# Performance work log

Measured on AMD Instinct MI355X. Metric: run time of the kernel, lower is better.

## Reference

```python
import jax, jax.numpy as jnp
import numpy as np

EPS = 0.05    # geomloss: blur**p with p=1, blur=0.05
NITER = 30    # fixed Sinkhorn iterations (geomloss uses eps-scaling; fixed-eps loop is the reference math)


def _cost(x, y):
    # x:(N,3), y:(M,3) -> (N,M) Euclidean distance (p=1 ground cost)
    d2 = jnp.sum((x[:, None, :] - y[None, :, :]) ** 2, axis=-1)
    return jnp.sqrt(d2 + 1e-12)


def _sinkhorn_ot(x, y):
    # Entropic OT cost between uniform measures on x (N pts) and y (M pts), log-domain Sinkhorn.
    n, m = x.shape[0], y.shape[0]
    C = _cost(x, y)                                  # (N,M)
    log_a = jnp.full((n,), -jnp.log(jnp.float32(n)), dtype=x.dtype)
    log_b = jnp.full((m,), -jnp.log(jnp.float32(m)), dtype=x.dtype)

    def step(carry, _):
        f, g = carry
        # f_i = -eps * LSE_j( log_b_j + (g_j - C_ij)/eps )
        f = -EPS * jax.nn.logsumexp(log_b[None, :] + (g[None, :] - C) / EPS, axis=1)
        g = -EPS * jax.nn.logsumexp(log_a[:, None] + (f[:, None] - C) / EPS, axis=0)
        return (f, g), None

    f0 = jnp.zeros((n,), dtype=x.dtype)
    g0 = jnp.zeros((m,), dtype=x.dtype)
    (f, g), _ = jax.lax.scan(step, (f0, g0), None, length=NITER)
    a = jnp.exp(log_a)
    b = jnp.exp(log_b)
    return jnp.sum(a * f) + jnp.sum(b * g)


def _sinkhorn_divergence(x, y):
    # Debiased Sinkhorn divergence: S(x,y) = OT(x,y) - 0.5*OT(x,x) - 0.5*OT(y,y)
    return _sinkhorn_ot(x, y) - 0.5 * _sinkhorn_ot(x, x) - 0.5 * _sinkhorn_ot(y, y)


def setup_inputs() -> dict:
    key = jax.random.key(0)
    k1, k2 = jax.random.split(key)
    B, N, M = 8, 2048, 2048
    xyz1 = jax.random.normal(k1, (B, N, 3), dtype=jnp.float32)
    xyz2 = jax.random.normal(k2, (B, M, 3), dtype=jnp.float32)
    return {"xyz1": xyz1, "xyz2": xyz2}


def reference(xyz1, xyz2):
    # Per-batch Sinkhorn divergence, averaged over batch (original loops over b; vmap is the
    # vectorized equivalent since clouds are independent).
    losses = jax.vmap(_sinkhorn_divergence)(xyz1, xyz2)   # (B,)
    return jnp.sum(losses) / xyz1.shape[0]
```

## Files before the change

kernel.cpp:

```cpp
#include <hip/hip_runtime.h>

#define NPTS    2048
#define NBATCH  8
#define NPROB   24
#define NITER   30
#define TPB     512
#define WPB     8
#define NJOBS   32
#define HCOLS   1024
#define CPW     128

constexpr float KSC = 28.853900817779268f;
constexpr float C1f = 0.38123094930796995f;
constexpr float C2f = 0.03465735902799726f;

typedef float v2f __attribute__((ext_vector_type(2)));

__device__ __forceinline__ float fexp2(float x) { return __builtin_amdgcn_exp2f(x); }
__device__ __forceinline__ float flog2(float x) { return __builtin_amdgcn_logf(x); }
__device__ __forceinline__ float fsqrt(float x) { return __builtin_amdgcn_sqrtf(x); }

__global__ __launch_bounds__(256)
void init_sums(float* __restrict__ gsum)
{
    int i = blockIdx.x * 256 + threadIdx.x;
    if (i < NPROB * 2 * NPTS) gsum[i] = 1024.0f;
}

__device__ __forceinline__ void problem_barrier(unsigned* arrive, unsigned* epoch,
                                                unsigned phase, int nbpp, int tid)
{
    __syncthreads();
    if (tid == 0) {
        unsigned old = __hip_atomic_fetch_add(arrive, 1u, __ATOMIC_ACQ_REL,
                                              __HIP_MEMORY_SCOPE_AGENT);
        if (old == (unsigned)(nbpp - 1)) {
            __hip_atomic_store(arrive, 0u, __ATOMIC_RELAXED, __HIP_MEMORY_SCOPE_AGENT);
            __hip_atomic_store(epoch, phase, __ATOMIC_RELEASE, __HIP_MEMORY_SCOPE_AGENT);
        } else {
            while (__hip_atomic_load(epoch, __ATOMIC_RELAXED,
                                     __HIP_MEMORY_SCOPE_AGENT) < phase) {
                __builtin_amdgcn_s_sleep(2);
            }
            __threadfence();
        }
    }
    __syncthreads();
}

__global__ __launch_bounds__(TPB, 6)
void sinkhorn_all(const float* __restrict__ xyz1,
                  const float* __restrict__ xyz2,
                  float* __restrict__ fsum,
                  float* __restrict__ gsum,
                  unsigned* __restrict__ bars,
                  int nbpp)
{
    __shared__ float4 shC[HCOLS];
    __shared__ float  shS[WPB][128];

    const int tid  = threadIdx.x;
    const int lane = tid & 63;
    const int warp = tid >> 6;
    const int p    = blockIdx.x % NPROB;
    const int lb   = blockIdx.x / NPROB;
    const int b    = p / 3;
    const int k    = p - 3 * b;

    const float* xb = xyz1 + (size_t)b * NPTS * 3;
    const float* yb = xyz2 + (size_t)b * NPTS * 3;
    float* fS = fsum + (size_t)p * 2 * NPTS;
    float* gS = gsum + (size_t)p * 2 * NPTS;
    unsigned* arrive = bars + (size_t)p * 64;
    unsigned* epoch  = bars + (size_t)p * 64 + 32;

    const float* Uf = (k == 2) ? yb : xb;
    const float* Ug = (k == 0) ? yb : ((k == 1) ? xb : yb);
    const float* Vf = (k == 1) ? xb : yb;
    const float* Vg = (k == 2) ? yb : xb;

    auto stage = [&](const float* __restrict__ V, const float* __restrict__ S, int h) {
        if (tid < 256) {
            const float4* V4 = (const float4*)V;
            const int i0 = 3 * (h * 256 + tid);
            const float4 a  = V4[i0 + 0];
            const float4 bb = V4[i0 + 1];
            const float4 cc = V4[i0 + 2];
            const int c  = 4 * tid;
            const int gc = h * HCOLS + c;
            const float4 t0 = *(const float4*)(S + gc);
            const float4 t1 = *(const float4*)(S + NPTS + gc);
            shC[c + 0] = make_float4(a.x,  a.y,  a.z,  11.0f - flog2(t0.x + t1.x));
            shC[c + 1] = make_float4(a.w,  bb.x, bb.y, 11.0f - flog2(t0.y + t1.y));
            shC[c + 2] = make_float4(bb.z, bb.w, cc.x, 11.0f - flog2(t0.z + t1.z));
            shC[c + 3] = make_float4(cc.y, cc.z, cc.w, 11.0f - flog2(t0.w + t1.w));
        }
    };

    auto do_pass = [&](const float* __restrict__ U, float* __restrict__ oS,
                       int h, int rc) {
        __syncthreads();
        const int r0 = rc * 128 + lane, r1 = r0 + 64;
        const v2f ux = {U[3*r0],   U[3*r1]};
        const v2f uy = {U[3*r0+1], U[3*r1+1]};
        const v2f uz = {U[3*r0+2], U[3*r1+2]};
        const v2f e12 = {1e-12f, 1e-12f};
        const v2f nK  = {-KSC, -KSC};
        v2f s0 = {0.f, 0.f}, s1 = {0.f, 0.f}, s2 = {0.f, 0.f}, s3 = {0.f, 0.f};

        auto term = [&](const float4 v) -> v2f {
            v2f dx = ux - (v2f){v.x, v.x};
            v2f dy = uy - (v2f){v.y, v.y};
            v2f dz = uz - (v2f){v.z, v.z};
            v2f d2 = __builtin_elementwise_fma(dz, dz, e12);
            d2 = __builtin_elementwise_fma(dy, dy, d2);
            d2 = __builtin_elementwise_fma(dx, dx, d2);
            v2f sq  = {fsqrt(d2.x), fsqrt(d2.y)};
            v2f arg = __builtin_elementwise_fma(nK, sq, (v2f){v.w, v.w});
            return (v2f){fexp2(arg.x), fexp2(arg.y)};
        };
        const int cb = warp * CPW;
        #pragma unroll 2
        for (int c = cb; c < cb + CPW; c += 4) {
            const float4 v0 = shC[c + 0];
            const float4 v1 = shC[c + 1];
            const float4 v2 = shC[c + 2];
            const float4 v3 = shC[c + 3];
            s0 += term(v0);
            s1 += term(v1);
            s2 += term(v2);
            s3 += term(v3);
        }
        shS[warp][lane]      = (s0.x + s1.x) + (s2.x + s3.x);
        shS[warp][lane + 64] = (s0.y + s1.y) + (s2.y + s3.y);
        __syncthreads();
        if (tid < 128) {
            float t = shS[0][tid];
            #pragma unroll
            for (int w = 1; w < WPB; ++w) t += shS[w][tid];
            oS[h * NPTS + rc * 128 + tid] = t;
        }
        __syncthreads();
    };

    for (int it = 0; it < NITER; ++it) {
        for (int j = lb; j < NJOBS; j += nbpp) {
            stage(Vf, gS, j & 1);
            do_pass(Uf, fS, j & 1, j >> 1);
        }
        problem_barrier(arrive, epoch, (unsigned)(2 * it + 1), nbpp, tid);
        for (int j = lb; j < NJOBS; j += nbpp) {
            stage(Vg, fS, j & 1);
            do_pass(Ug, gS, j & 1, j >> 1);
        }
        problem_barrier(arrive, epoch, (unsigned)(2 * it + 2), nbpp, tid);
    }
}

__global__ __launch_bounds__(TPB, 1)
void final_reduce(const float* __restrict__ fsum, const float* __restrict__ gsum,
                  float* __restrict__ out)
{
    __shared__ double red[WPB];
    const int tid  = threadIdx.x;
    const int lane = tid & 63;
    const int warp = tid >> 6;

    double acc = 0.0;
    for (int idx = tid; idx < 2 * NPROB * NPTS; idx += TPB) {
        const bool isF = idx < NPROB * NPTS;
        const int rem  = isF ? idx : idx - NPROB * NPTS;
        const int pp   = rem >> 11;
        const int j    = rem & (NPTS - 1);
        const float* S = (isF ? fsum : gsum) + (size_t)pp * 2 * NPTS;
        const float t  = S[j] + S[NPTS + j];
        const float val = C1f - C2f * flog2(t);
        const float w   = (pp % 3 == 0) ? 1.0f : -0.5f;
        acc += (double)val * (double)w;
    }
    #pragma unroll
    for (int off = 32; off > 0; off >>= 1) acc += __shfl_xor(acc, off);
    if (lane == 0) red[warp] = acc;
    __syncthreads();
    if (warp == 0) {
        double v2 = (lane < WPB) ? red[lane] : 0.0;
        #pragma unroll
        for (int off = 32; off > 0; off >>= 1) v2 += __shfl_xor(v2, off);
        if (lane == 0) out[0] = (float)(v2 / (double)(NBATCH * NPTS));
    }
}

extern "C" void kernel_launch(void* const* d_in, const int* in_sizes, int n_in,
                              void* d_out, int out_size, void* d_ws, size_t ws_size,
                              hipStream_t stream)
{
    const float* xyz1 = (const float*)d_in[0];
    const float* xyz2 = (const float*)d_in[1];
    float* out = (float*)d_out;

    float* fsum = (float*)d_ws;
    float* gsum = fsum + (size_t)NPROB * 2 * NPTS;
    unsigned* bars = (unsigned*)(gsum + (size_t)NPROB * 2 * NPTS);

    hipMemsetAsync(bars, 0, (size_t)NPROB * 64 * sizeof(unsigned), stream);
    init_sums<<<(NPROB * 2 * NPTS + 255) / 256, 256, 0, stream>>>(gsum);

    int maxB = 0;
    hipOccupancyMaxActiveBlocksPerMultiprocessor(&maxB, sinkhorn_all, TPB, 0);
    if (maxB < 1) maxB = 1;
    int bpp = (maxB * 256) / NPROB;
    if (bpp > NJOBS) bpp = NJOBS;
    if (bpp < 1) bpp = 1;
    int nblk = NPROB * bpp;

    void* args[] = { (void*)&xyz1, (void*)&xyz2, (void*)&fsum, (void*)&gsum,
                     (void*)&bars, (void*)&bpp };
    hipLaunchCooperativeKernel((void*)sinkhorn_all, dim3(nblk), dim3(TPB),
                               args, 0, stream);

    final_reduce<<<1, TPB, 0, stream>>>(fsum, gsum, out);
}
```

Before: 2.349 ms.

## Split column range into four partial-sum quarters to raise block count per problem

Generalizes the column split from halves to a runtime-selected number of quarters (4 when workspace allows), doubling the number of jobs per Sinkhorn half-step, and raises the launch-bounds minimum-blocks hint from 6 to 8. The aim is to give more blocks work per problem so more of the GPU is used between grid-level barriers. In exchange, each stage step reads and sums more partial-sum arrays, does more staging and reduction per unit of compute, and the launch-bounds change may constrain registers.

```diff
diff --git a/kernel.cpp b/kernel.cpp
--- a/kernel.cpp
+++ b/kernel.cpp
@@ -6,9 +6,6 @@
 #define NITER   30
 #define TPB     512
 #define WPB     8
-#define NJOBS   32
-#define HCOLS   1024
-#define CPW     128
 
 constexpr float KSC = 28.853900817779268f;
 constexpr float C1f = 0.38123094930796995f;
@@ -21,10 +18,10 @@
 __device__ __forceinline__ float fsqrt(float x) { return __builtin_amdgcn_sqrtf(x); }
 
 __global__ __launch_bounds__(256)
-void init_sums(float* __restrict__ gsum)
+void init_sums(float* __restrict__ gsum, int n, float val)
 {
     int i = blockIdx.x * 256 + threadIdx.x;
-    if (i < NPROB * 2 * NPTS) gsum[i] = 1024.0f;
+    if (i < n) gsum[i] = val;
 }
 
 __device__ __forceinline__ void problem_barrier(unsigned* arrive, unsigned* epoch,
@@ -48,16 +45,21 @@
     __syncthreads();
 }
 
-__global__ __launch_bounds__(TPB, 6)
+__global__ __launch_bounds__(TPB, 8)
 void sinkhorn_all(const float* __restrict__ xyz1,
                   const float* __restrict__ xyz2,
                   float* __restrict__ fsum,
                   float* __restrict__ gsum,
                   unsigned* __restrict__ bars,
-                  int nbpp)
-{
-    __shared__ float4 shC[HCOLS];
+                  int nbpp, int lognq)
+{
+    __shared__ float4 shC[1024];
     __shared__ float  shS[WPB][128];
+
+    const int nq    = 1 << lognq;
+    const int njobs = 16 << lognq;
+    const int hc    = NPTS >> lognq;
+    const int cpw   = hc >> 3;
 
     const int tid  = threadIdx.x;
     const int lane = tid & 63;
@@ -69,8 +71,8 @@
 
     const float* xb = xyz1 + (size_t)b * NPTS * 3;
     const float* yb = xyz2 + (size_t)b * NPTS * 3;
-    float* fS = fsum + (size_t)p * 2 * NPTS;
-    float* gS = gsum + (size_t)p * 2 * NPTS;
+    float* fS = fsum + (size_t)p * nq * NPTS;
+    float* gS = gsum + (size_t)p * nq * NPTS;
     unsigned* arrive = bars + (size_t)p * 64;
     unsigned* epoch  = bars + (size_t)p * 64 + 32;
 
@@ -79,26 +81,30 @@
     const float* Vf = (k == 1) ? xb : yb;
     const float* Vg = (k == 2) ? yb : xb;
 
-    auto stage = [&](const float* __restrict__ V, const float* __restrict__ S, int h) {
-        if (tid < 256) {
+    auto stage = [&](const float* __restrict__ V, const float* __restrict__ S, int q) {
+        const int nst = hc >> 2;
+        if (tid < nst) {
             const float4* V4 = (const float4*)V;
-            const int i0 = 3 * (h * 256 + tid);
+            const int g0 = q * hc + 4 * tid;
+            const int i0 = 3 * (g0 >> 2);
             const float4 a  = V4[i0 + 0];
             const float4 bb = V4[i0 + 1];
             const float4 cc = V4[i0 + 2];
-            const int c  = 4 * tid;
-            const int gc = h * HCOLS + c;
-            const float4 t0 = *(const float4*)(S + gc);
-            const float4 t1 = *(const float4*)(S + NPTS + gc);
-            shC[c + 0] = make_float4(a.x,  a.y,  a.z,  11.0f - flog2(t0.x + t1.x));
-            shC[c + 1] = make_float4(a.w,  bb.x, bb.y, 11.0f - flog2(t0.y + t1.y));
-            shC[c + 2] = make_float4(bb.z, bb.w, cc.x, 11.0f - flog2(t0.z + t1.z));
-            shC[c + 3] = make_float4(cc.y, cc.z, cc.w, 11.0f - flog2(t0.w + t1.w));
+            float4 ts = *(const float4*)(S + g0);
+            for (int qq = 1; qq < nq; ++qq) {
+                const float4 t = *(const float4*)(S + qq * NPTS + g0);
+                ts.x += t.x; ts.y += t.y; ts.z += t.z; ts.w += t.w;
+            }
+            const int c = 4 * tid;
+            shC[c + 0] = make_float4(a.x,  a.y,  a.z,  11.0f - flog2(ts.x));
+            shC[c + 1] = make_float4(a.w,  bb.x, bb.y, 11.0f - flog2(ts.y));
+            shC[c + 2] = make_float4(bb.z, bb.w, cc.x, 11.0f - flog2(ts.z));
+            shC[c + 3] = make_float4(cc.y, cc.z, cc.w, 11.0f - flog2(ts.w));
         }
     };
 
     auto do_pass = [&](const float* __restrict__ U, float* __restrict__ oS,
-                       int h, int rc) {
+                       int q, int rc) {
         __syncthreads();
         const int r0 = rc * 128 + lane, r1 = r0 + 64;
         const v2f ux = {U[3*r0],   U[3*r1]};
@@ -119,9 +125,9 @@
             v2f arg = __builtin_elementwise_fma(nK, sq, (v2f){v.w, v.w});
             return (v2f){fexp2(arg.x), fexp2(arg.y)};
         };
-        const int cb = warp * CPW;
+        const int cb = warp * cpw;
         #pragma unroll 2
-        for (int c = cb; c < cb + CPW; c += 4) {
+        for (int c = cb; c < cb + cpw; c += 4) {
             const float4 v0 = shC[c + 0];
             const float4 v1 = shC[c + 1];
             const float4 v2 = shC[c + 2];
@@ -138,20 +144,20 @@
             float t = shS[0][tid];
             #pragma unroll
             for (int w = 1; w < WPB; ++w) t += shS[w][tid];
-            oS[h * NPTS + rc * 128 + tid] = t;
+            oS[q * NPTS + rc * 128 + tid] = t;
         }
         __syncthreads();
     };
 
     for (int it = 0; it < NITER; ++it) {
-        for (int j = lb; j < NJOBS; j += nbpp) {
-            stage(Vf, gS, j & 1);
-            do_pass(Uf, fS, j & 1, j >> 1);
+        for (int j = lb; j < njobs; j += nbpp) {
+            stage(Vf, gS, j & (nq - 1));
+            do_pass(Uf, fS, j & (nq - 1), j >> lognq);
         }
         problem_barrier(arrive, epoch, (unsigned)(2 * it + 1), nbpp, tid);
-        for (int j = lb; j < NJOBS; j += nbpp) {
-            stage(Vg, fS, j & 1);
-            do_pass(Ug, gS, j & 1, j >> 1);
+        for (int j = lb; j < njobs; j += nbpp) {
+            stage(Vg, fS, j & (nq - 1));
+            do_pass(Ug, gS, j & (nq - 1), j >> lognq);
         }
         problem_barrier(arrive, epoch, (unsigned)(2 * it + 2), nbpp, tid);
     }
@@ -159,9 +165,10 @@
 
 __global__ __launch_bounds__(TPB, 1)
 void final_reduce(const float* __restrict__ fsum, const float* __restrict__ gsum,
-                  float* __restrict__ out)
+                  float* __restrict__ out, int lognq)
 {
     __shared__ double red[WPB];
+    const int nq   = 1 << lognq;
     const int tid  = threadIdx.x;
     const int lane = tid & 63;
     const int warp = tid >> 6;
@@ -172,8 +179,9 @@
         const int rem  = isF ? idx : idx - NPROB * NPTS;
         const int pp   = rem >> 11;
         const int j    = rem & (NPTS - 1);
-        const float* S = (isF ? fsum : gsum) + (size_t)pp * 2 * NPTS;
-        const float t  = S[j] + S[NPTS + j];
+        const float* S = (isF ? fsum : gsum) + (size_t)pp * nq * NPTS;
+        float t = S[j];
+        for (int q = 1; q < nq; ++q) t += S[q * NPTS + j];
         const float val = C1f - C2f * flog2(t);
         const float w   = (pp % 3 == 0) ? 1.0f : -0.5f;
         acc += (double)val * (double)w;
@@ -198,25 +206,33 @@
     const float* xyz2 = (const float*)d_in[1];
     float* out = (float*)d_out;
 
+    size_t need4 = (size_t)NPROB * 4 * NPTS * sizeof(float) * 2
+                 + (size_t)NPROB * 64 * sizeof(unsigned);
+    int lognq = (ws_size >= need4) ? 2 : 1;
+    int nq    = 1 << lognq;
+    int njobs = 16 << lognq;
+
     float* fsum = (float*)d_ws;
-    float* gsum = fsum + (size_t)NPROB * 2 * NPTS;
-    unsigned* bars = (unsigned*)(gsum + (size_t)NPROB * 2 * NPTS);
+    float* gsum = fsum + (size_t)NPROB * nq * NPTS;
+    unsigned* bars = (unsigned*)(gsum + (size_t)NPROB * nq * NPTS);
 
     hipMemsetAsync(bars, 0, (size_t)NPROB * 64 * sizeof(unsigned), stream);
-    init_sums<<<(NPROB * 2 * NPTS + 255) / 256, 256, 0, stream>>>(gsum);
+    int ninit = NPROB * nq * NPTS;
+    init_sums<<<(ninit + 255) / 256, 256, 0, stream>>>(gsum, ninit,
+                                                       (float)(NPTS / nq));
 
     int maxB = 0;
     hipOccupancyMaxActiveBlocksPerMultiprocessor(&maxB, sinkhorn_all, TPB, 0);
     if (maxB < 1) maxB = 1;
     int bpp = (maxB * 256) / NPROB;
-    if (bpp > NJOBS) bpp = NJOBS;
+    if (bpp > njobs) bpp = njobs;
     if (bpp < 1) bpp = 1;
     int nblk = NPROB * bpp;
 
     void* args[] = { (void*)&xyz1, (void*)&xyz2, (void*)&fsum, (void*)&gsum,
-                     (void*)&bars, (void*)&bpp };
+                     (void*)&bars, (void*)&bpp, (void*)&lognq };
     hipLaunchCooperativeKernel((void*)sinkhorn_all, dim3(nblk), dim3(TPB),
                                args, 0, stream);
 
-    final_reduce<<<1, TPB, 0, stream>>>(fsum, gsum, out);
-}
+    final_reduce<<<1, TPB, 0, stream>>>(fsum, gsum, out, lognq);
+}
```

Measured after the change: 2.513 ms. 1.07x slower.
